# Performance work log

Measured on AMD Instinct MI355X. Metric: run time of the kernel, lower is better.

The kernel has to match this reference:

```python
import math
import jax, jax.numpy as jnp
import numpy as np

QUERY_DIM = 768
FEAT_DIM = 1024
HID_DIM = 768
OUT_DIM = 768
B, L, S, T = 32, 256, 64, 64


def _linear_params(key, fan_in, fan_out):
    kw, kb = jax.random.split(key)
    scale = 1.0 / math.sqrt(fan_in)
    W = jax.random.uniform(kw, (fan_in, fan_out), jnp.float32, -scale, scale)
    b = jax.random.uniform(kb, (fan_out,), jnp.float32, -scale, scale)
    return W, b


def setup_inputs() -> dict:
    key = jax.random.key(0)
    ks = jax.random.split(key, 7)
    query = jax.random.normal(ks[0], (B, L, QUERY_DIM), jnp.float32)
    src = jax.random.normal(ks[1], (B, S, FEAT_DIM), jnp.float32)
    trg = jax.random.normal(ks[2], (B, T, FEAT_DIM), jnp.float32)
    Wq, b_q = _linear_params(ks[3], QUERY_DIM, HID_DIM)
    Ws, b_s = _linear_params(ks[4], FEAT_DIM, HID_DIM)
    Wt, b_t = _linear_params(ks[5], FEAT_DIM, HID_DIM)
    Wo, b_o = _linear_params(ks[6], HID_DIM + QUERY_DIM, OUT_DIM)
    return {"query": query, "src": src, "trg": trg,
            "Wq": Wq, "b_q": b_q, "Ws": Ws, "b_s": b_s,
            "Wt": Wt, "b_t": b_t, "Wo": Wo, "b_o": b_o}


def reference(query, src, trg, Wq, b_q, Ws, b_s, Wt, b_t, Wo, b_o):
    # Projections (LinearAct with identity activation).
    q = query @ Wq + b_q          # (b, l, h)
    s_key = src @ Ws + b_s        # (b, s, h)
    t_key = trg @ Wt + b_t        # (b, t, h)
    # rel_key[b, t, s, h] = tanh(s_key[b, s, h] + t_key[b, t, h])
    rel_key = jnp.tanh(s_key[:, None, :, :] + t_key[:, :, None, :])  # (b, t, s, h)
    # Scores over combined (t, s) positions.
    weight = jnp.einsum('blk,btsk->blts', q, rel_key) / math.sqrt(HID_DIM)  # (b, l, t, s)
    b_, l_, t_, s_ = weight.shape
    weight = jax.nn.softmax(weight.reshape(b_, l_, t_ * s_), axis=-1).reshape(b_, l_, t_, s_)
    # Context: weighted sum of rel_key over (t, s).
    rel_ctx = jnp.einsum('blts,btsk->blk', weight, rel_key)  # (b, l, h)
    x = jnp.concatenate([query, rel_ctx], axis=-1)           # (b, l, h + q)
    return jax.nn.relu(x @ Wo + b_o)                          # (b, l, out)
```

## Files before the change

### kernel.cpp

```cpp
#include <hip/hip_runtime.h>
#include <math.h>


typedef __attribute__((ext_vector_type(8))) short bf16x8;
typedef __attribute__((ext_vector_type(4))) float f32x4;

__device__ __forceinline__ unsigned short f2bf(float f) {
    union { float f; unsigned u; } x; x.f = f;
    unsigned u = x.u;
    return (unsigned short)((u + 0x7fffu + ((u >> 16) & 1u)) >> 16);
}
__device__ __forceinline__ float bf2f(unsigned short h) {
    union { unsigned u; float f; } x; x.u = (unsigned)h << 16;
    return x.f;
}
__device__ __forceinline__ float tanh_fast(float x) {
    float e = __expf(2.0f * x);
    return 1.0f - 2.0f * __builtin_amdgcn_rcpf(1.0f + e);
}
__device__ __forceinline__ void async_copy16(void* lds, const void* g) {
    __builtin_amdgcn_global_load_lds(
        (const __attribute__((address_space(1))) unsigned int*)g,
        (__attribute__((address_space(3))) unsigned int*)lds,
        16, 0, 0);
}

template<bool OUT_BF16, bool RELU>
__global__ __launch_bounds__(256, 2) void gemm_bt_kernel(
    const unsigned short* __restrict__ A, const unsigned short* __restrict__ BT,
    void* __restrict__ Cout, const float* __restrict__ bias,
    int M, int N, int K, int lda, int ldb, int ldc,
    long long sA, long long sB, long long sC)
{
    __shared__ unsigned short As[128 * 32];
    __shared__ unsigned short Bs[128 * 32];
    const int z = blockIdx.z;
    A  += (long long)z * sA;
    BT += (long long)z * sB;
    const int m0 = blockIdx.x * 128, n0 = blockIdx.y * 128;
    const int tid = threadIdx.x;
    const int lane = tid & 63, wid = tid >> 6;
    const int wr = wid >> 1, wc = wid & 1;
    const int r = lane & 15, g = lane >> 4;

    f32x4 acc[4][4] = {};

    for (int k0 = 0; k0 < K; k0 += 32) {
        __syncthreads();
        #pragma unroll
        for (int j = 0; j < 2; ++j) {
            int c = j * 256 + tid;
            int row = c >> 2, kc = (c & 3) * 8;
            async_copy16(&As[c * 8], A  + (size_t)(m0 + row) * lda + k0 + kc);
            async_copy16(&Bs[c * 8], BT + (size_t)(n0 + row) * ldb + k0 + kc);
        }
        asm volatile("s_waitcnt vmcnt(0)" ::: "memory");
        __syncthreads();

        bf16x8 af[4], bfr[4];
        #pragma unroll
        for (int m = 0; m < 4; ++m)
            af[m] = *(const bf16x8*)&As[(wr * 64 + m * 16 + r) * 32 + g * 8];
        #pragma unroll
        for (int n = 0; n < 4; ++n)
            bfr[n] = *(const bf16x8*)&Bs[(wc * 64 + n * 16 + r) * 32 + g * 8];
        #pragma unroll
        for (int m = 0; m < 4; ++m)
            #pragma unroll
            for (int n = 0; n < 4; ++n)
                acc[m][n] = __builtin_amdgcn_mfma_f32_16x16x32_bf16(
                    af[m], bfr[n], acc[m][n], 0, 0, 0);
    }

    float* Cf = (float*)Cout;
    unsigned short* Cb = (unsigned short*)Cout;
    const long long cbase = (long long)z * sC;
    #pragma unroll
    for (int n = 0; n < 4; ++n) {
        int col = n0 + wc * 64 + n * 16 + r;
        float bv = bias ? bias[col] : 0.0f;
        #pragma unroll
        for (int m = 0; m < 4; ++m) {
            int row0 = m0 + wr * 64 + m * 16 + g * 4;
            #pragma unroll
            for (int i = 0; i < 4; ++i) {
                float v = acc[m][n][i] + bv;
                if (RELU) v = fmaxf(v, 0.0f);
                size_t off = (size_t)cbase + (size_t)(row0 + i) * ldc + col;
                if (OUT_BF16) Cb[off] = f2bf(v);
                else          Cf[off] = v;
            }
        }
    }
}

__global__ __launch_bounds__(256, 2) void scores_kernel(
    const unsigned short* __restrict__ qh,
    const float* __restrict__ s_key,
    const float* __restrict__ t_key,
    unsigned short* __restrict__ scores)
{
    __shared__ unsigned short As[128 * 32];
    __shared__ unsigned short Bs[128 * 40];
    __shared__ float Sk[64 * 36];
    __shared__ float Tk[2 * 32];

    const int b = blockIdx.z;
    const unsigned short* A = qh + (size_t)b * 256 * 768;
    const float* skp = s_key + (size_t)b * 64 * 768;
    const float* tkp = t_key + (size_t)b * 64 * 768;
    const int m0 = blockIdx.x * 128, n0 = blockIdx.y * 128;
    const int t0 = n0 >> 6;
    const int tid = threadIdx.x;
    const int lane = tid & 63, wid = tid >> 6;
    const int wr = wid >> 1, wc = wid & 1;
    const int r = lane & 15, g = lane >> 4;

    f32x4 acc[4][4] = {};

    for (int k0 = 0; k0 < 768; k0 += 32) {
        __syncthreads();
        if (tid < 64) Tk[tid] = tkp[(size_t)(t0 + (tid >> 5)) * 768 + k0 + (tid & 31)];
        #pragma unroll
        for (int j = 0; j < 2; ++j) {
            int c = j * 256 + tid;
            int row = c >> 2, kc = (c & 3) * 8;
            async_copy16(&As[c * 8], A + (size_t)(m0 + row) * 768 + k0 + kc);
        }
        {
            int s = tid >> 2, c4 = (tid & 3) * 8;
            float4 v0 = *(const float4*)&skp[(size_t)s * 768 + k0 + c4];
            float4 v1 = *(const float4*)&skp[(size_t)s * 768 + k0 + c4 + 4];
            *(float4*)&Sk[s * 36 + c4]     = v0;
            *(float4*)&Sk[s * 36 + c4 + 4] = v1;
        }
        asm volatile("s_waitcnt vmcnt(0)" ::: "memory");
        __syncthreads();

        #pragma unroll
        for (int j = 0; j < 2; ++j) {
            int c = j * 256 + tid;
            int n = c >> 2, kc = (c & 3) * 8;
            const float* sv = &Sk[(n & 63) * 36 + kc];
            const float* tv = &Tk[(n >> 6) * 32 + kc];
            bf16x8 o;
            #pragma unroll
            for (int e = 0; e < 8; ++e)
                o[e] = (short)f2bf(tanh_fast(sv[e] + tv[e]));
            *(bf16x8*)&Bs[n * 40 + kc] = o;
        }
        __syncthreads();

        bf16x8 af[4], bfr[4];
        #pragma unroll
        for (int m = 0; m < 4; ++m)
            af[m] = *(const bf16x8*)&As[(wr * 64 + m * 16 + r) * 32 + g * 8];
        #pragma unroll
        for (int n = 0; n < 4; ++n)
            bfr[n] = *(const bf16x8*)&Bs[(wc * 64 + n * 16 + r) * 40 + g * 8];
        #pragma unroll
        for (int m = 0; m < 4; ++m)
            #pragma unroll
            for (int n = 0; n < 4; ++n)
                acc[m][n] = __builtin_amdgcn_mfma_f32_16x16x32_bf16(
                    af[m], bfr[n], acc[m][n], 0, 0, 0);
    }

    unsigned short* C = scores + (size_t)b * 256 * 4096;
    #pragma unroll
    for (int n = 0; n < 4; ++n) {
        int col = n0 + wc * 64 + n * 16 + r;
        #pragma unroll
        for (int m = 0; m < 4; ++m) {
            int row0 = m0 + wr * 64 + m * 16 + g * 4;
            #pragma unroll
            for (int i = 0; i < 4; ++i)
                C[(size_t)(row0 + i) * 4096 + col] = f2bf(acc[m][n][i]);
        }
    }
}

__global__ __launch_bounds__(256, 2) void ctx_kernel(
    const unsigned short* __restrict__ w,
    const float* __restrict__ s_key,
    const float* __restrict__ t_key,
    unsigned short* __restrict__ xcat)
{
    __shared__ unsigned short As[128 * 32];
    __shared__ unsigned short Bs[128 * 40];
    __shared__ float Sk[64 * 132];

    const int b = blockIdx.z;
    const unsigned short* A = w + (size_t)b * 256 * 4096;
    const float* skp = s_key + (size_t)b * 64 * 768;
    const float* tkp = t_key + (size_t)b * 64 * 768;
    const int m0 = blockIdx.x * 128, n0 = blockIdx.y * 128;
    const int tid = threadIdx.x;
    const int lane = tid & 63, wid = tid >> 6;
    const int wr = wid >> 1, wc = wid & 1;
    const int r = lane & 15, g = lane >> 4;

    #pragma unroll
    for (int it = 0; it < 8; ++it) {
        int idx = it * 256 + tid;
        int s = idx >> 5, c4 = (idx & 31) * 4;
        *(float4*)&Sk[s * 132 + c4] = *(const float4*)&skp[(size_t)s * 768 + n0 + c4];
    }

    const int sl = tid & 31;
    const int hq = tid >> 5;

    f32x4 acc[4][4] = {};
    __syncthreads();

    for (int k0 = 0; k0 < 4096; k0 += 32) {
        const int t = k0 >> 6, s0 = k0 & 63;
        __syncthreads();
        #pragma unroll
        for (int j = 0; j < 2; ++j) {
            int c = j * 256 + tid;
            int row = c >> 2, kc = (c & 3) * 8;
            async_copy16(&As[c * 8], A + (size_t)(m0 + row) * 4096 + k0 + kc);
        }
        #pragma unroll
        for (int j = 0; j < 2; ++j) {
            int h0 = (j * 8 + hq) * 8;
            int s = s0 + sl;
            float4 sa = *(const float4*)&Sk[s * 132 + h0];
            float4 sb = *(const float4*)&Sk[s * 132 + h0 + 4];
            float4 ta = *(const float4*)&tkp[(size_t)t * 768 + n0 + h0];
            float4 tb = *(const float4*)&tkp[(size_t)t * 768 + n0 + h0 + 4];
            unsigned short o0 = f2bf(tanh_fast(sa.x + ta.x));
            unsigned short o1 = f2bf(tanh_fast(sa.y + ta.y));
            unsigned short o2 = f2bf(tanh_fast(sa.z + ta.z));
            unsigned short o3 = f2bf(tanh_fast(sa.w + ta.w));
            unsigned short o4 = f2bf(tanh_fast(sb.x + tb.x));
            unsigned short o5 = f2bf(tanh_fast(sb.y + tb.y));
            unsigned short o6 = f2bf(tanh_fast(sb.z + tb.z));
            unsigned short o7 = f2bf(tanh_fast(sb.w + tb.w));
            Bs[(h0 + 0) * 40 + sl] = o0;
            Bs[(h0 + 1) * 40 + sl] = o1;
            Bs[(h0 + 2) * 40 + sl] = o2;
            Bs[(h0 + 3) * 40 + sl] = o3;
            Bs[(h0 + 4) * 40 + sl] = o4;
            Bs[(h0 + 5) * 40 + sl] = o5;
            Bs[(h0 + 6) * 40 + sl] = o6;
            Bs[(h0 + 7) * 40 + sl] = o7;
        }
        asm volatile("s_waitcnt vmcnt(0)" ::: "memory");
        __syncthreads();

        bf16x8 af[4], bfr[4];
        #pragma unroll
        for (int m = 0; m < 4; ++m)
            af[m] = *(const bf16x8*)&As[(wr * 64 + m * 16 + r) * 32 + g * 8];
        #pragma unroll
        for (int n = 0; n < 4; ++n)
            bfr[n] = *(const bf16x8*)&Bs[(wc * 64 + n * 16 + r) * 40 + g * 8];
        #pragma unroll
        for (int m = 0; m < 4; ++m)
            #pragma unroll
            for (int n = 0; n < 4; ++n)
                acc[m][n] = __builtin_amdgcn_mfma_f32_16x16x32_bf16(
                    af[m], bfr[n], acc[m][n], 0, 0, 0);
    }

    unsigned short* C = xcat + (size_t)b * 256 * 1536 + 768;
    #pragma unroll
    for (int n = 0; n < 4; ++n) {
        int col = n0 + wc * 64 + n * 16 + r;
        #pragma unroll
        for (int m = 0; m < 4; ++m) {
            int row0 = m0 + wr * 64 + m * 16 + g * 4;
            #pragma unroll
            for (int i = 0; i < 4; ++i)
                C[(size_t)(row0 + i) * 1536 + col] = f2bf(acc[m][n][i]);
        }
    }
}

__global__ void cvt_bf16_kernel(const float* __restrict__ in,
                                unsigned short* __restrict__ out, int n4) {
    int i = blockIdx.x * 256 + threadIdx.x;
    if (i >= n4) return;
    float4 v = ((const float4*)in)[i];
    ushort4 o;
    o.x = f2bf(v.x); o.y = f2bf(v.y); o.z = f2bf(v.z); o.w = f2bf(v.w);
    ((ushort4*)out)[i] = o;
}

__global__ void cvt_query_kernel(const float* __restrict__ in,
                                 unsigned short* __restrict__ xcat) {
    int i = blockIdx.x * 256 + threadIdx.x;
    if (i >= 8192 * 192) return;
    int row = i / 192, c4 = (i % 192) * 4;
    float4 v = ((const float4*)in)[i];
    ushort4 o;
    o.x = f2bf(v.x); o.y = f2bf(v.y); o.z = f2bf(v.z); o.w = f2bf(v.w);
    *(ushort4*)&xcat[(size_t)row * 1536 + c4] = o;
}

__global__ void transpose_w_kernel(const float* __restrict__ in,
                                   unsigned short* __restrict__ out,
                                   int R, int C) {
    __shared__ float tile[64][65];
    const int r0 = blockIdx.y * 64, c0 = blockIdx.x * 64;
    const int tx = threadIdx.x & 63, ty = threadIdx.x >> 6;
    for (int i = ty; i < 64; i += 4)
        tile[i][tx] = in[(size_t)(r0 + i) * C + c0 + tx];
    __syncthreads();
    for (int i = ty; i < 64; i += 4)
        out[(size_t)(c0 + i) * R + r0 + tx] = f2bf(tile[tx][i]);
}

__global__ __launch_bounds__(256) void softmax_kernel(unsigned short* __restrict__ scores) {
    unsigned short* p = scores + (size_t)blockIdx.x * 4096;
    const int tid = threadIdx.x, lane = tid & 63, wid = tid >> 6;
    __shared__ float red[4];

    float v[16];
    {
        const bf16x8* p8 = (const bf16x8*)p;
        bf16x8 a = p8[tid * 2], c = p8[tid * 2 + 1];
        #pragma unroll
        for (int e = 0; e < 8; ++e) {
            v[e]     = bf2f((unsigned short)a[e]);
            v[8 + e] = bf2f((unsigned short)c[e]);
        }
    }
    float mx = v[0];
    #pragma unroll
    for (int e = 1; e < 16; ++e) mx = fmaxf(mx, v[e]);
    #pragma unroll
    for (int o = 32; o; o >>= 1) mx = fmaxf(mx, __shfl_xor(mx, o));
    if (lane == 0) red[wid] = mx;
    __syncthreads();
    mx = fmaxf(fmaxf(red[0], red[1]), fmaxf(red[2], red[3]));
    __syncthreads();

    const float scale = 0.03608439182435161f;
    float sum = 0.0f;
    #pragma unroll
    for (int e = 0; e < 16; ++e) {
        v[e] = __expf((v[e] - mx) * scale);
        sum += v[e];
    }
    #pragma unroll
    for (int o = 32; o; o >>= 1) sum += __shfl_xor(sum, o);
    if (lane == 0) red[wid] = sum;
    __syncthreads();
    sum = red[0] + red[1] + red[2] + red[3];
    const float inv = 1.0f / sum;

    bf16x8* p8 = (bf16x8*)p;
    #pragma unroll
    for (int j = 0; j < 2; ++j) {
        bf16x8 o;
        #pragma unroll
        for (int e = 0; e < 8; ++e)
            o[e] = (short)f2bf(v[j * 8 + e] * inv);
        p8[tid * 2 + j] = o;
    }
}

extern "C" void kernel_launch(void* const* d_in, const int* in_sizes, int n_in,
                              void* d_out, int out_size, void* d_ws, size_t ws_size,
                              hipStream_t stream) {
    const float* query = (const float*)d_in[0];
    const float* src   = (const float*)d_in[1];
    const float* trg   = (const float*)d_in[2];
    const float* Wq    = (const float*)d_in[3];
    const float* b_q   = (const float*)d_in[4];
    const float* Ws    = (const float*)d_in[5];
    const float* b_s   = (const float*)d_in[6];
    const float* Wt    = (const float*)d_in[7];
    const float* b_t   = (const float*)d_in[8];
    const float* Wo    = (const float*)d_in[9];
    const float* b_o   = (const float*)d_in[10];

    char* ws = (char*)d_ws;
    size_t off = 0;
    auto alloc = [&](size_t bytes) {
        void* p = ws + off;
        off += (bytes + 255) & ~(size_t)255;
        return p;
    };
    unsigned short* xcat   = (unsigned short*)alloc((size_t)8192 * 1536 * 2);
    unsigned short* srcbf  = (unsigned short*)alloc((size_t)2048 * 1024 * 2);
    unsigned short* trgbf  = (unsigned short*)alloc((size_t)2048 * 1024 * 2);
    unsigned short* WqT    = (unsigned short*)alloc((size_t)768 * 768 * 2);
    unsigned short* WsT    = (unsigned short*)alloc((size_t)768 * 1024 * 2);
    unsigned short* WtT    = (unsigned short*)alloc((size_t)768 * 1024 * 2);
    unsigned short* WoT    = (unsigned short*)alloc((size_t)768 * 1536 * 2);
    unsigned short* qh     = (unsigned short*)alloc((size_t)8192 * 768 * 2);
    float*          s_key  = (float*)alloc((size_t)2048 * 768 * 4);
    float*          t_key  = (float*)alloc((size_t)2048 * 768 * 4);
    unsigned short* scores = (unsigned short*)alloc((size_t)32 * 256 * 4096 * 2);

    cvt_query_kernel<<<6144, 256, 0, stream>>>(query, xcat);
    cvt_bf16_kernel<<<2048, 256, 0, stream>>>(src, srcbf, 524288);
    cvt_bf16_kernel<<<2048, 256, 0, stream>>>(trg, trgbf, 524288);

    transpose_w_kernel<<<dim3(12, 12), 256, 0, stream>>>(Wq, WqT, 768, 768);
    transpose_w_kernel<<<dim3(12, 16), 256, 0, stream>>>(Ws, WsT, 1024, 768);
    transpose_w_kernel<<<dim3(12, 16), 256, 0, stream>>>(Wt, WtT, 1024, 768);
    transpose_w_kernel<<<dim3(12, 24), 256, 0, stream>>>(Wo, WoT, 1536, 768);

    gemm_bt_kernel<true, false><<<dim3(64, 6, 1), 256, 0, stream>>>(
        xcat, WqT, qh, b_q, 8192, 768, 768, 1536, 768, 768, 0, 0, 0);
    gemm_bt_kernel<false, false><<<dim3(16, 6, 1), 256, 0, stream>>>(
        srcbf, WsT, s_key, b_s, 2048, 768, 1024, 1024, 1024, 768, 0, 0, 0);
    gemm_bt_kernel<false, false><<<dim3(16, 6, 1), 256, 0, stream>>>(
        trgbf, WtT, t_key, b_t, 2048, 768, 1024, 1024, 1024, 768, 0, 0, 0);

    scores_kernel<<<dim3(2, 32, 32), 256, 0, stream>>>(qh, s_key, t_key, scores);

    softmax_kernel<<<8192, 256, 0, stream>>>(scores);

    ctx_kernel<<<dim3(2, 6, 32), 256, 0, stream>>>(scores, s_key, t_key, xcat);

    gemm_bt_kernel<false, true><<<dim3(64, 6, 1), 256, 0, stream>>>(
        xcat, WoT, d_out, b_o, 8192, 768, 1536, 1536, 1536, 768, 0, 0, 0);
}
```

Before: 513.8 us.

## Halve ctx_kernel N-tile, drop s_key LDS staging, double grid

The ctx_kernel N-tile shrinks from 128 to 64 hidden columns, so the grid doubles to 768 blocks, and launch bounds rise to 3 blocks per CU. The s_key slice is no longer staged in LDS; each thread reads s_key and t_key straight from global memory every k-step and builds its tanh tile with half the work. The goal is more blocks and occupancy to cover the 256 CUs and less LDS per block. The cost is that each A tile of softmax weights is now loaded by twice as many blocks, and the s_key reads go to global memory on every iteration.

Result: slower. 524.1 us (+2.0%).

```diff
diff --git a/kernel.cpp b/kernel.cpp
--- a/kernel.cpp
+++ b/kernel.cpp
@@ -180,41 +180,30 @@
     }
 }
 
-__global__ __launch_bounds__(256, 2) void ctx_kernel(
+__global__ __launch_bounds__(256, 3) void ctx_kernel(
     const unsigned short* __restrict__ w,
     const float* __restrict__ s_key,
     const float* __restrict__ t_key,
     unsigned short* __restrict__ xcat)
 {
     __shared__ unsigned short As[128 * 32];
-    __shared__ unsigned short Bs[128 * 40];
-    __shared__ float Sk[64 * 132];
+    __shared__ unsigned short Bs[64 * 40];
 
     const int b = blockIdx.z;
     const unsigned short* A = w + (size_t)b * 256 * 4096;
     const float* skp = s_key + (size_t)b * 64 * 768;
     const float* tkp = t_key + (size_t)b * 64 * 768;
-    const int m0 = blockIdx.x * 128, n0 = blockIdx.y * 128;
+    const int m0 = blockIdx.x * 128, n0 = blockIdx.y * 64;
     const int tid = threadIdx.x;
     const int lane = tid & 63, wid = tid >> 6;
     const int wr = wid >> 1, wc = wid & 1;
     const int r = lane & 15, g = lane >> 4;
-
-    #pragma unroll
-    for (int it = 0; it < 8; ++it) {
-        int idx = it * 256 + tid;
-        int s = idx >> 5, c4 = (idx & 31) * 4;
-        *(float4*)&Sk[s * 132 + c4] = *(const float4*)&skp[(size_t)s * 768 + n0 + c4];
-    }
-
-    const int sl = tid & 31;
-    const int hq = tid >> 5;
-
-    f32x4 acc[4][4] = {};
-    __syncthreads();
+    const int sl = tid & 31, hg = tid >> 5;
+
+    f32x4 acc[4][2] = {};
 
     for (int k0 = 0; k0 < 4096; k0 += 32) {
-        const int t = k0 >> 6, s0 = k0 & 63;
+        const int t = k0 >> 6, s = (k0 & 63) + sl;
         __syncthreads();
         #pragma unroll
         for (int j = 0; j < 2; ++j) {
@@ -222,53 +211,42 @@
             int row = c >> 2, kc = (c & 3) * 8;
             async_copy16(&As[c * 8], A + (size_t)(m0 + row) * 4096 + k0 + kc);
         }
-        #pragma unroll
-        for (int j = 0; j < 2; ++j) {
-            int h0 = (j * 8 + hq) * 8;
-            int s = s0 + sl;
-            float4 sa = *(const float4*)&Sk[s * 132 + h0];
-            float4 sb = *(const float4*)&Sk[s * 132 + h0 + 4];
-            float4 ta = *(const float4*)&tkp[(size_t)t * 768 + n0 + h0];
-            float4 tb = *(const float4*)&tkp[(size_t)t * 768 + n0 + h0 + 4];
-            unsigned short o0 = f2bf(tanh_fast(sa.x + ta.x));
-            unsigned short o1 = f2bf(tanh_fast(sa.y + ta.y));
-            unsigned short o2 = f2bf(tanh_fast(sa.z + ta.z));
-            unsigned short o3 = f2bf(tanh_fast(sa.w + ta.w));
-            unsigned short o4 = f2bf(tanh_fast(sb.x + tb.x));
-            unsigned short o5 = f2bf(tanh_fast(sb.y + tb.y));
-            unsigned short o6 = f2bf(tanh_fast(sb.z + tb.z));
-            unsigned short o7 = f2bf(tanh_fast(sb.w + tb.w));
-            Bs[(h0 + 0) * 40 + sl] = o0;
-            Bs[(h0 + 1) * 40 + sl] = o1;
-            Bs[(h0 + 2) * 40 + sl] = o2;
-            Bs[(h0 + 3) * 40 + sl] = o3;
-            Bs[(h0 + 4) * 40 + sl] = o4;
-            Bs[(h0 + 5) * 40 + sl] = o5;
-            Bs[(h0 + 6) * 40 + sl] = o6;
-            Bs[(h0 + 7) * 40 + sl] = o7;
+        {
+            const float* sv = &skp[(size_t)s * 768 + n0 + hg * 8];
+            const float* tv = &tkp[(size_t)t * 768 + n0 + hg * 8];
+            float4 sa = *(const float4*)sv, sb = *(const float4*)(sv + 4);
+            float4 ta = *(const float4*)tv, tb = *(const float4*)(tv + 4);
+            Bs[(hg * 8 + 0) * 40 + sl] = f2bf(tanh_fast(sa.x + ta.x));
+            Bs[(hg * 8 + 1) * 40 + sl] = f2bf(tanh_fast(sa.y + ta.y));
+            Bs[(hg * 8 + 2) * 40 + sl] = f2bf(tanh_fast(sa.z + ta.z));
+            Bs[(hg * 8 + 3) * 40 + sl] = f2bf(tanh_fast(sa.w + ta.w));
+            Bs[(hg * 8 + 4) * 40 + sl] = f2bf(tanh_fast(sb.x + tb.x));
+            Bs[(hg * 8 + 5) * 40 + sl] = f2bf(tanh_fast(sb.y + tb.y));
+            Bs[(hg * 8 + 6) * 40 + sl] = f2bf(tanh_fast(sb.z + tb.z));
+            Bs[(hg * 8 + 7) * 40 + sl] = f2bf(tanh_fast(sb.w + tb.w));
         }
         asm volatile("s_waitcnt vmcnt(0)" ::: "memory");
         __syncthreads();
 
-        bf16x8 af[4], bfr[4];
+        bf16x8 af[4], bfr[2];
         #pragma unroll
         for (int m = 0; m < 4; ++m)
             af[m] = *(const bf16x8*)&As[(wr * 64 + m * 16 + r) * 32 + g * 8];
         #pragma unroll
-        for (int n = 0; n < 4; ++n)
-            bfr[n] = *(const bf16x8*)&Bs[(wc * 64 + n * 16 + r) * 40 + g * 8];
-        #pragma unroll
-        for (int m = 0; m < 4; ++m)
-            #pragma unroll
-            for (int n = 0; n < 4; ++n)
+        for (int n = 0; n < 2; ++n)
+            bfr[n] = *(const bf16x8*)&Bs[(wc * 32 + n * 16 + r) * 40 + g * 8];
+        #pragma unroll
+        for (int m = 0; m < 4; ++m)
+            #pragma unroll
+            for (int n = 0; n < 2; ++n)
                 acc[m][n] = __builtin_amdgcn_mfma_f32_16x16x32_bf16(
                     af[m], bfr[n], acc[m][n], 0, 0, 0);
     }
 
     unsigned short* C = xcat + (size_t)b * 256 * 1536 + 768;
     #pragma unroll
-    for (int n = 0; n < 4; ++n) {
-        int col = n0 + wc * 64 + n * 16 + r;
+    for (int n = 0; n < 2; ++n) {
+        int col = n0 + wc * 32 + n * 16 + r;
         #pragma unroll
         for (int m = 0; m < 4; ++m) {
             int row0 = m0 + wr * 64 + m * 16 + g * 4;
@@ -417,7 +395,7 @@
 
     softmax_kernel<<<8192, 256, 0, stream>>>(scores);
 
-    ctx_kernel<<<dim3(2, 6, 32), 256, 0, stream>>>(scores, s_key, t_key, xcat);
+    ctx_kernel<<<dim3(2, 12, 32), 256, 0, stream>>>(scores, s_key, t_key, xcat);
 
     gemm_bt_kernel<false, true><<<dim3(64, 6, 1), 256, 0, stream>>>(
         xcat, WoT, d_out, b_o, 8192, 768, 1536, 1536, 1536, 768, 0, 0, 0);
```
